# Kernel optimization log

Measured on AMD Instinct MI355X. Metric: run time of the kernel, lower is better.

The kernel has to match this reference:

```python
import jax, jax.numpy as jnp
import numpy as np


def setup_inputs() -> dict:
    key = jax.random.key(0)
    kq, kk, kv = jax.random.split(key, 3)
    B, H, N, D = 2, 16, 2048, 64
    q = jax.random.normal(kq, (B, H, N, D), dtype=jnp.float32)
    k = jax.random.normal(kk, (B, H, N, D), dtype=jnp.float32)
    v = jax.random.normal(kv, (B, H, N, D), dtype=jnp.float32)
    return {"q": q, "k": k, "v": v}


def reference(q, k, v):
    # RBF-kernel causal attention: logits = -relu(||q-k||^2) / sqrt(D)
    B, H, N, D = q.shape
    sm_scale = 1.0 / jnp.sqrt(jnp.asarray(D, dtype=q.dtype))
    q_sq = jnp.sum(q * q, axis=-1)              # [B,H,N]
    k_sq = jnp.sum(k * k, axis=-1)              # [B,H,N]
    qk = jnp.einsum("bhmd,bhnd->bhmn", q, k)    # [B,H,N,N]
    dist_sq = q_sq[..., :, None] + k_sq[..., None, :] - 2.0 * qk
    dist_sq = jnp.maximum(dist_sq, 0.0)         # relu on squared distance
    logits = -dist_sq * sm_scale
    # causal mask: query m attends to keys n <= m
    causal = jnp.tril(jnp.ones((N, N), dtype=bool))
    logits = jnp.where(causal, logits, -jnp.inf)
    p = jax.nn.softmax(logits, axis=-1)
    out = jnp.einsum("bhmn,bhnd->bhmd", p, v)
    return out
```

## Files before the change

kernel.cpp:

```cpp
#include <hip/hip_runtime.h>

#define NN 2048
#define DD 64
#define C1 0.36067376f
#define C1H 0.18033688f

typedef _Float16 h8 __attribute__((ext_vector_type(8)));
typedef _Float16 h4 __attribute__((ext_vector_type(4)));
typedef float f32x16 __attribute__((ext_vector_type(16)));

union H8U4 { h8 v; unsigned u[4]; };

__global__ __launch_bounds__(256) void prep(const float* __restrict__ k,
                                            const float* __restrict__ v,
                                            _Float16* __restrict__ Ks,
                                            _Float16* __restrict__ Vs,
                                            float* __restrict__ hk) {
    __shared__ _Float16 T[128][72];
    const int tb = blockIdx.x, bh = blockIdx.y, tid = threadIdx.x;
    const size_t ibase = (size_t)bh * NN * DD + (size_t)tb * 128 * DD;
    const int lane = tid & 63, ln = lane & 31, lh = lane >> 5;

#pragma unroll
    for (int it = 0; it < 8; ++it) {
        int f = tid + 256 * it;
        int row = f >> 4, c4 = (f & 15) * 4;
        float4 a = *(const float4*)&k[ibase + (size_t)row * DD + c4];
        h4 hv = {(_Float16)a.x, (_Float16)a.y, (_Float16)a.z, (_Float16)a.w};
        *(h4*)&T[row][c4] = hv;
        float s = a.x * a.x + a.y * a.y + a.z * a.z + a.w * a.w;
        s += __shfl_xor(s, 1, 16);
        s += __shfl_xor(s, 2, 16);
        s += __shfl_xor(s, 4, 16);
        s += __shfl_xor(s, 8, 16);
        if ((tid & 15) == 0) hk[bh * NN + tb * 128 + row] = s * C1H;
    }
    __syncthreads();
#pragma unroll
    for (int it = 0; it < 4; ++it) {
        int f2 = tid + 256 * it;
        int combo = f2 >> 6;
        int jl = combo >> 2, c = combo & 3;
        h8 r = *(const h8*)&T[32 * jl + ln][16 * c + 8 * lh];
        *(h8*)&Ks[(size_t)bh * 131072 + (size_t)(4 * tb + jl) * 2048
                  + (size_t)(c * 64 + lane) * 8] = r;
    }
    __syncthreads();

#pragma unroll
    for (int it = 0; it < 8; ++it) {
        int f = tid + 256 * it;
        int row = f >> 4, c4 = (f & 15) * 4;
        float4 a = *(const float4*)&v[ibase + (size_t)row * DD + c4];
        h4 hv = {(_Float16)a.x, (_Float16)a.y, (_Float16)a.z, (_Float16)a.w};
        *(h4*)&T[row][c4] = hv;
    }
    __syncthreads();
#pragma unroll
    for (int it = 0; it < 4; ++it) {
        int f2 = tid + 256 * it;
        int combo = f2 >> 6;
        int jl = combo >> 2, o = (combo >> 1) & 1, c = combo & 1;
        h8 r;
#pragma unroll
        for (int jx = 0; jx < 8; ++jx)
            r[jx] = T[32 * jl + 16 * c + 8 * lh + jx][32 * o + ln];
        *(h8*)&Vs[(size_t)bh * 131072 + (size_t)(4 * tb + jl) * 2048
                  + (size_t)(o * 128 + c * 64 + lane) * 8] = r;
    }
}

__global__ __launch_bounds__(128, 2) void rbf_attn(
    const float* __restrict__ q, const _Float16* __restrict__ Ks,
    const _Float16* __restrict__ Vs, const float* __restrict__ hk,
    float* __restrict__ out)
{
    const int tid = threadIdx.x;
    const int bh = blockIdx.x;
    const int qb = 31 - blockIdx.y;
    const int wv = tid >> 6, lane = tid & 63;
    const int ln = lane & 31, lh = lane >> 5;
    const int jmax = 2 * qb + wv;
    const int qrow = qb * 64 + wv * 32 + ln;
    const size_t fbase = (size_t)bh * NN * DD;

    h8 qf[4];
    {
        const float* qr = q + fbase + (size_t)qrow * DD;
#pragma unroll
        for (int c = 0; c < 4; ++c) {
            float4 a = *(const float4*)&qr[16 * c + 8 * lh];
            float4 b = *(const float4*)&qr[16 * c + 8 * lh + 4];
            qf[c] = h8{(_Float16)a.x, (_Float16)a.y, (_Float16)a.z, (_Float16)a.w,
                       (_Float16)b.x, (_Float16)b.y, (_Float16)b.z, (_Float16)b.w};
        }
    }

    const _Float16* Ksb = Ks + (size_t)bh * 131072;
    const _Float16* Vsb = Vs + (size_t)bh * 131072;
    const float4* hk4 = (const float4*)(hk + bh * NN);
    const int klq = (lh * 32 + ln) * 8;

    f32x16 O0, O1;
#pragma unroll
    for (int r = 0; r < 16; ++r) { O0[r] = 0.f; O1[r] = 0.f; }
    float lsum = 0.f, mrun = -INFINITY;

    auto loadT = [&](int jj, h8 (&kf)[4], h8 (&vf)[4], float4 (&hr)[4]) {
        const _Float16* kp = Ksb + (size_t)jj * 2048 + klq;
        const _Float16* vp = Vsb + (size_t)jj * 2048 + klq;
#pragma unroll
        for (int c = 0; c < 4; ++c) kf[c] = *(const h8*)(kp + c * 512);
#pragma unroll
        for (int oc = 0; oc < 4; ++oc)
            vf[oc] = *(const h8*)(vp + (oc >> 1) * 1024 + (oc & 1) * 512);
#pragma unroll
        for (int g = 0; g < 4; ++g) hr[g] = hk4[jj * 8 + g * 2 + lh];
    };

    auto comp = [&](int jj, h8 (&kf)[4], h8 (&vf)[4], float4 (&hr)[4]) {
        f32x16 S;
#pragma unroll
        for (int r = 0; r < 16; ++r) S[r] = 0.f;
#pragma unroll
        for (int c = 0; c < 4; ++c)
            S = __builtin_amdgcn_mfma_f32_32x32x16_f16(kf[c], qf[c], S, 0, 0, 0);

        const bool diag = (jj == jmax);
        float x[16];
#pragma unroll
        for (int r = 0; r < 16; ++r) {
            const float* hf = (const float*)&hr[r >> 2];
            float xv = fmaf(S[r], C1, -hf[r & 3]);
            if (diag) {
                int keyloc = (r & 3) + 8 * (r >> 2) + 4 * lh;
                if (keyloc > ln) xv = -INFINITY;
            }
            x[r] = xv;
        }
        float mt = x[0];
#pragma unroll
        for (int r = 1; r < 16; ++r) mt = fmaxf(mt, x[r]);
        mt = fmaxf(mt, __shfl_xor(mt, 32));
        if (__ballot(mt > mrun) != 0ull) {
            float mnew = fmaxf(mrun, mt);
            float alpha = __builtin_amdgcn_exp2f(mrun - mnew);
            mrun = mnew;
            lsum *= alpha;
#pragma unroll
            for (int r = 0; r < 16; ++r) { O0[r] *= alpha; O1[r] *= alpha; }
        }
        float p[16], ps = 0.f;
#pragma unroll
        for (int r = 0; r < 16; ++r) {
            p[r] = __builtin_amdgcn_exp2f(x[r] - mrun);
            ps += p[r];
        }
        lsum += ps;

        unsigned pk[8];
#pragma unroll
        for (int hh = 0; hh < 8; ++hh) {
            auto pr = __builtin_amdgcn_cvt_pkrtz(p[2 * hh], p[2 * hh + 1]);
            unsigned pu; __builtin_memcpy(&pu, &pr, 4);
            pk[hh] = pu;
        }
#pragma unroll
        for (int s = 0; s < 2; ++s) {
            unsigned send0 = lh ? pk[4 * s + 0] : pk[4 * s + 2];
            unsigned send1 = lh ? pk[4 * s + 1] : pk[4 * s + 3];
            unsigned r0 = (unsigned)__shfl_xor((int)send0, 32);
            unsigned r1 = (unsigned)__shfl_xor((int)send1, 32);
            H8U4 pb;
            pb.u[0] = lh ? r0 : pk[4 * s + 0];
            pb.u[1] = lh ? r1 : pk[4 * s + 1];
            pb.u[2] = lh ? pk[4 * s + 2] : r0;
            pb.u[3] = lh ? pk[4 * s + 3] : r1;
            O0 = __builtin_amdgcn_mfma_f32_32x32x16_f16(vf[s], pb.v, O0, 0, 0, 0);
            O1 = __builtin_amdgcn_mfma_f32_32x32x16_f16(vf[2 + s], pb.v, O1, 0, 0, 0);
        }
    };

    h8 kfA[4], vfA[4]; float4 hrA[4];
    h8 kfB[4], vfB[4]; float4 hrB[4];
    loadT(0, kfA, vfA, hrA);
    __builtin_amdgcn_sched_barrier(0);
    int jj = 0;
    while (true) {
        if (jj < jmax) loadT(jj + 1, kfB, vfB, hrB);
        __builtin_amdgcn_sched_barrier(0);
        comp(jj, kfA, vfA, hrA);
        __builtin_amdgcn_sched_barrier(0);
        if (++jj > jmax) break;
        if (jj < jmax) loadT(jj + 1, kfA, vfA, hrA);
        __builtin_amdgcn_sched_barrier(0);
        comp(jj, kfB, vfB, hrB);
        __builtin_amdgcn_sched_barrier(0);
        if (++jj > jmax) break;
    }

    float lt = lsum + __shfl_xor(lsum, 32);
    float inv = 1.f / lt;
    size_t ro = fbase + (size_t)qrow * DD;
#pragma unroll
    for (int g = 0; g < 4; ++g) {
        float4 o0 = make_float4(O0[4 * g + 0] * inv, O0[4 * g + 1] * inv,
                                O0[4 * g + 2] * inv, O0[4 * g + 3] * inv);
        *(float4*)&out[ro + 8 * g + 4 * lh] = o0;
        float4 o1 = make_float4(O1[4 * g + 0] * inv, O1[4 * g + 1] * inv,
                                O1[4 * g + 2] * inv, O1[4 * g + 3] * inv);
        *(float4*)&out[ro + 32 + 8 * g + 4 * lh] = o1;
    }
}

extern "C" void kernel_launch(void* const* d_in, const int* in_sizes, int n_in,
                              void* d_out, int out_size, void* d_ws, size_t ws_size,
                              hipStream_t stream) {
    (void)in_sizes; (void)n_in; (void)out_size; (void)ws_size;
    const float* q = (const float*)d_in[0];
    const float* k = (const float*)d_in[1];
    const float* v = (const float*)d_in[2];
    float* out = (float*)d_out;

    float* hk = (float*)d_ws;
    _Float16* Ks = (_Float16*)((char*)d_ws + 262144);
    _Float16* Vs = (_Float16*)((char*)d_ws + 262144 + 8388608);

    prep<<<dim3(16, 32), 256, 0, stream>>>(k, v, Ks, Vs, hk);
    rbf_attn<<<dim3(32, 32), 128, 0, stream>>>(q, Ks, Vs, hk, out);
}
```

Before: 138.4 us.

## Fuse prep and attention into cooperative kernel with grid sync and asm loads

Merges the K/V fp16 conversion prep kernel and the attention kernel into one cooperative launch. Each block prepares a 64-row slice, then all blocks meet at a grid-wide sync before attention, which removes one kernel launch and the gap between launches. Tile loads now go through inline-asm global_load_dwordx4 with explicit vmcnt waits in place of compiler-scheduled loads and sched barriers. The risks are the cost of the grid barrier, the need for all 1024 blocks to be co-resident, and a fallback to two launches if the cooperative launch fails.

```diff
diff --git a/kernel.cpp b/kernel.cpp
--- a/kernel.cpp
+++ b/kernel.cpp
@@ -1,4 +1,7 @@
 #include <hip/hip_runtime.h>
+#include <hip/hip_cooperative_groups.h>
+
+namespace cg = cooperative_groups;
 
 #define NN 2048
 #define DD 64
@@ -7,49 +10,54 @@
 
 typedef _Float16 h8 __attribute__((ext_vector_type(8)));
 typedef _Float16 h4 __attribute__((ext_vector_type(4)));
+typedef float fx4 __attribute__((ext_vector_type(4)));
 typedef float f32x16 __attribute__((ext_vector_type(16)));
 
-union H8U4 { h8 v; unsigned u[4]; };
-
-__global__ __launch_bounds__(256) void prep(const float* __restrict__ k,
-                                            const float* __restrict__ v,
-                                            _Float16* __restrict__ Ks,
-                                            _Float16* __restrict__ Vs,
-                                            float* __restrict__ hk) {
-    __shared__ _Float16 T[128][72];
-    const int tb = blockIdx.x, bh = blockIdx.y, tid = threadIdx.x;
-    const size_t ibase = (size_t)bh * NN * DD + (size_t)tb * 128 * DD;
-    const int lane = tid & 63, ln = lane & 31, lh = lane >> 5;
-
+#define GL4(dst, ap, off) \
+    asm volatile("global_load_dwordx4 %0, %1, off offset:" off \
+                 : "=v"(dst) : "v"(ap))
+
+#define WAITS(cnt, K, V, H) \
+    asm volatile("s_waitcnt vmcnt(" cnt ")" \
+        : "+v"(K[0]), "+v"(K[1]), "+v"(K[2]), "+v"(K[3]), \
+          "+v"(V[0]), "+v"(V[1]), "+v"(V[2]), "+v"(V[3]), \
+          "+v"(H[0]), "+v"(H[1]), "+v"(H[2]), "+v"(H[3]))
+
+__device__ __forceinline__ void prep_phase(
+    int bh, int s, int tid,
+    const float* __restrict__ k, const float* __restrict__ v,
+    _Float16* __restrict__ Ks, _Float16* __restrict__ Vs,
+    float* __restrict__ hkw, _Float16 (*T)[72])
+{
+    const size_t ibase = (size_t)bh * NN * DD + (size_t)s * 64 * DD;
 #pragma unroll
     for (int it = 0; it < 8; ++it) {
-        int f = tid + 256 * it;
+        int f = tid + 128 * it;
         int row = f >> 4, c4 = (f & 15) * 4;
         float4 a = *(const float4*)&k[ibase + (size_t)row * DD + c4];
         h4 hv = {(_Float16)a.x, (_Float16)a.y, (_Float16)a.z, (_Float16)a.w};
         *(h4*)&T[row][c4] = hv;
-        float s = a.x * a.x + a.y * a.y + a.z * a.z + a.w * a.w;
-        s += __shfl_xor(s, 1, 16);
-        s += __shfl_xor(s, 2, 16);
-        s += __shfl_xor(s, 4, 16);
-        s += __shfl_xor(s, 8, 16);
-        if ((tid & 15) == 0) hk[bh * NN + tb * 128 + row] = s * C1H;
+        float sq = a.x * a.x + a.y * a.y + a.z * a.z + a.w * a.w;
+        sq += __shfl_xor(sq, 1, 16);
+        sq += __shfl_xor(sq, 2, 16);
+        sq += __shfl_xor(sq, 4, 16);
+        sq += __shfl_xor(sq, 8, 16);
+        if ((tid & 15) == 0) hkw[bh * NN + s * 64 + row] = sq * C1H;
     }
     __syncthreads();
 #pragma unroll
     for (int it = 0; it < 4; ++it) {
-        int f2 = tid + 256 * it;
-        int combo = f2 >> 6;
-        int jl = combo >> 2, c = combo & 3;
-        h8 r = *(const h8*)&T[32 * jl + ln][16 * c + 8 * lh];
-        *(h8*)&Ks[(size_t)bh * 131072 + (size_t)(4 * tb + jl) * 2048
-                  + (size_t)(c * 64 + lane) * 8] = r;
+        int rec = tid + 128 * it;
+        int tl = rec >> 8, c = (rec >> 6) & 3, lr = rec & 63;
+        int lnr = lr & 31, lhr = lr >> 5;
+        h8 r = *(const h8*)&T[32 * tl + lnr][16 * c + 8 * lhr];
+        *(h8*)&Ks[(size_t)bh * 131072 + (size_t)(s * 2 + tl) * 2048
+                  + (size_t)(c * 64 + lr) * 8] = r;
     }
     __syncthreads();
-
 #pragma unroll
     for (int it = 0; it < 8; ++it) {
-        int f = tid + 256 * it;
+        int f = tid + 128 * it;
         int row = f >> 4, c4 = (f & 15) * 4;
         float4 a = *(const float4*)&v[ibase + (size_t)row * DD + c4];
         h4 hv = {(_Float16)a.x, (_Float16)a.y, (_Float16)a.z, (_Float16)a.w};
@@ -58,26 +66,24 @@
     __syncthreads();
 #pragma unroll
     for (int it = 0; it < 4; ++it) {
-        int f2 = tid + 256 * it;
-        int combo = f2 >> 6;
-        int jl = combo >> 2, o = (combo >> 1) & 1, c = combo & 1;
+        int rec = tid + 128 * it;
+        int tl = rec >> 8, o = (rec >> 7) & 1, c = (rec >> 6) & 1, lr = rec & 63;
+        int lnr = lr & 31, lhr = lr >> 5;
         h8 r;
 #pragma unroll
         for (int jx = 0; jx < 8; ++jx)
-            r[jx] = T[32 * jl + 16 * c + 8 * lh + jx][32 * o + ln];
-        *(h8*)&Vs[(size_t)bh * 131072 + (size_t)(4 * tb + jl) * 2048
-                  + (size_t)(o * 128 + c * 64 + lane) * 8] = r;
-    }
-}
-
-__global__ __launch_bounds__(128, 2) void rbf_attn(
+            r[jx] = T[32 * tl + 16 * c + 8 * lhr + jx][32 * o + lnr];
+        *(h8*)&Vs[(size_t)bh * 131072 + (size_t)(s * 2 + tl) * 2048
+                  + (size_t)(o * 128 + c * 64 + lr) * 8] = r;
+    }
+}
+
+__device__ __forceinline__ void attn_phase(
+    int bh, int qb, int tid,
     const float* __restrict__ q, const _Float16* __restrict__ Ks,
-    const _Float16* __restrict__ Vs, const float* __restrict__ hk,
+    const _Float16* __restrict__ Vs, const float* __restrict__ hkw,
     float* __restrict__ out)
 {
-    const int tid = threadIdx.x;
-    const int bh = blockIdx.x;
-    const int qb = 31 - blockIdx.y;
     const int wv = tid >> 6, lane = tid & 63;
     const int ln = lane & 31, lh = lane >> 5;
     const int jmax = 2 * qb + wv;
@@ -96,51 +102,50 @@
         }
     }
 
-    const _Float16* Ksb = Ks + (size_t)bh * 131072;
-    const _Float16* Vsb = Vs + (size_t)bh * 131072;
-    const float4* hk4 = (const float4*)(hk + bh * NN);
-    const int klq = (lh * 32 + ln) * 8;
+    const unsigned long long kb0 =
+        (unsigned long long)Ks + (size_t)bh * 262144 + (size_t)lane * 16;
+    const unsigned long long vb0 =
+        (unsigned long long)Vs + (size_t)bh * 262144 + (size_t)lane * 16;
+    const unsigned long long hb0 =
+        (unsigned long long)(hkw + bh * NN) + (size_t)lh * 16;
 
     f32x16 O0, O1;
 #pragma unroll
     for (int r = 0; r < 16; ++r) { O0[r] = 0.f; O1[r] = 0.f; }
     float lsum = 0.f, mrun = -INFINITY;
 
-    auto loadT = [&](int jj, h8 (&kf)[4], h8 (&vf)[4], float4 (&hr)[4]) {
-        const _Float16* kp = Ksb + (size_t)jj * 2048 + klq;
-        const _Float16* vp = Vsb + (size_t)jj * 2048 + klq;
-#pragma unroll
-        for (int c = 0; c < 4; ++c) kf[c] = *(const h8*)(kp + c * 512);
-#pragma unroll
-        for (int oc = 0; oc < 4; ++oc)
-            vf[oc] = *(const h8*)(vp + (oc >> 1) * 1024 + (oc & 1) * 512);
-#pragma unroll
-        for (int g = 0; g < 4; ++g) hr[g] = hk4[jj * 8 + g * 2 + lh];
-    };
-
-    auto comp = [&](int jj, h8 (&kf)[4], h8 (&vf)[4], float4 (&hr)[4]) {
+#define ISSUE(jjv, K, V, H) do { \
+        unsigned long long kp = kb0 + (unsigned long long)(jjv) * 4096; \
+        unsigned long long vp = vb0 + (unsigned long long)(jjv) * 4096; \
+        unsigned long long hp = hb0 + (unsigned long long)(jjv) * 128;  \
+        GL4(K[0], kp, "0"); GL4(K[1], kp, "1024"); \
+        GL4(K[2], kp, "2048"); GL4(K[3], kp, "3072"); \
+        GL4(V[0], vp, "0"); GL4(V[1], vp, "1024"); \
+        GL4(V[2], vp, "2048"); GL4(V[3], vp, "3072"); \
+        GL4(H[0], hp, "0"); GL4(H[1], hp, "32"); \
+        GL4(H[2], hp, "64"); GL4(H[3], hp, "96"); \
+    } while (0)
+
+    auto comp = [&](int jj, fx4 (&K)[4], fx4 (&V)[4], fx4 (&H)[4]) {
         f32x16 S;
 #pragma unroll
         for (int r = 0; r < 16; ++r) S[r] = 0.f;
 #pragma unroll
-        for (int c = 0; c < 4; ++c)
-            S = __builtin_amdgcn_mfma_f32_32x32x16_f16(kf[c], qf[c], S, 0, 0, 0);
-
+        for (int c = 0; c < 4; ++c) {
+            h8 kf; __builtin_memcpy(&kf, &K[c], 16);
+            S = __builtin_amdgcn_mfma_f32_32x32x16_f16(kf, qf[c], S, 0, 0, 0);
+        }
         const bool diag = (jj == jmax);
-        float x[16];
 #pragma unroll
         for (int r = 0; r < 16; ++r) {
-            const float* hf = (const float*)&hr[r >> 2];
-            float xv = fmaf(S[r], C1, -hf[r & 3]);
-            if (diag) {
-                int keyloc = (r & 3) + 8 * (r >> 2) + 4 * lh;
-                if (keyloc > ln) xv = -INFINITY;
-            }
-            x[r] = xv;
-        }
-        float mt = x[0];
-#pragma unroll
-        for (int r = 1; r < 16; ++r) mt = fmaxf(mt, x[r]);
+            float hv = ((const float*)&H[r >> 2])[r & 3];
+            float xv = fmaf(S[r], C1, -hv);
+            if (diag && ((r & 3) + 8 * (r >> 2) + 4 * lh > ln)) xv = -INFINITY;
+            S[r] = xv;
+        }
+        float mt = S[0];
+#pragma unroll
+        for (int r = 1; r < 16; ++r) mt = fmaxf(mt, S[r]);
         mt = fmaxf(mt, __shfl_xor(mt, 32));
         if (__ballot(mt > mrun) != 0ull) {
             float mnew = fmaxf(mrun, mt);
@@ -150,54 +155,51 @@
 #pragma unroll
             for (int r = 0; r < 16; ++r) { O0[r] *= alpha; O1[r] *= alpha; }
         }
-        float p[16], ps = 0.f;
-#pragma unroll
-        for (int r = 0; r < 16; ++r) {
-            p[r] = __builtin_amdgcn_exp2f(x[r] - mrun);
-            ps += p[r];
-        }
-        lsum += ps;
-
         unsigned pk[8];
+        float ps = 0.f;
 #pragma unroll
         for (int hh = 0; hh < 8; ++hh) {
-            auto pr = __builtin_amdgcn_cvt_pkrtz(p[2 * hh], p[2 * hh + 1]);
+            float p0 = __builtin_amdgcn_exp2f(S[2 * hh] - mrun);
+            float p1 = __builtin_amdgcn_exp2f(S[2 * hh + 1] - mrun);
+            ps += p0 + p1;
+            auto pr = __builtin_amdgcn_cvt_pkrtz(p0, p1);
             unsigned pu; __builtin_memcpy(&pu, &pr, 4);
             pk[hh] = pu;
         }
+        lsum += ps;
 #pragma unroll
         for (int s = 0; s < 2; ++s) {
             unsigned send0 = lh ? pk[4 * s + 0] : pk[4 * s + 2];
             unsigned send1 = lh ? pk[4 * s + 1] : pk[4 * s + 3];
             unsigned r0 = (unsigned)__shfl_xor((int)send0, 32);
             unsigned r1 = (unsigned)__shfl_xor((int)send1, 32);
-            H8U4 pb;
-            pb.u[0] = lh ? r0 : pk[4 * s + 0];
-            pb.u[1] = lh ? r1 : pk[4 * s + 1];
-            pb.u[2] = lh ? pk[4 * s + 2] : r0;
-            pb.u[3] = lh ? pk[4 * s + 3] : r1;
-            O0 = __builtin_amdgcn_mfma_f32_32x32x16_f16(vf[s], pb.v, O0, 0, 0, 0);
-            O1 = __builtin_amdgcn_mfma_f32_32x32x16_f16(vf[2 + s], pb.v, O1, 0, 0, 0);
+            unsigned pb[4];
+            pb[0] = lh ? r0 : pk[4 * s + 0];
+            pb[1] = lh ? r1 : pk[4 * s + 1];
+            pb[2] = lh ? pk[4 * s + 2] : r0;
+            pb[3] = lh ? pk[4 * s + 3] : r1;
+            h8 pbv; __builtin_memcpy(&pbv, pb, 16);
+            h8 v0; __builtin_memcpy(&v0, &V[s], 16);
+            h8 v1; __builtin_memcpy(&v1, &V[2 + s], 16);
+            O0 = __builtin_amdgcn_mfma_f32_32x32x16_f16(v0, pbv, O0, 0, 0, 0);
+            O1 = __builtin_amdgcn_mfma_f32_32x32x16_f16(v1, pbv, O1, 0, 0, 0);
         }
     };
 
-    h8 kfA[4], vfA[4]; float4 hrA[4];
-    h8 kfB[4], vfB[4]; float4 hrB[4];
-    loadT(0, kfA, vfA, hrA);
-    __builtin_amdgcn_sched_barrier(0);
+    fx4 KA[4], VA[4], HA[4], KB[4], VB[4], HB[4];
+    ISSUE(0, KA, VA, HA);
     int jj = 0;
     while (true) {
-        if (jj < jmax) loadT(jj + 1, kfB, vfB, hrB);
-        __builtin_amdgcn_sched_barrier(0);
-        comp(jj, kfA, vfA, hrA);
-        __builtin_amdgcn_sched_barrier(0);
+        if (jj < jmax) { ISSUE(jj + 1, KB, VB, HB); WAITS("12", KA, VA, HA); }
+        else           { WAITS("0", KA, VA, HA); }
+        comp(jj, KA, VA, HA);
         if (++jj > jmax) break;
-        if (jj < jmax) loadT(jj + 1, kfA, vfA, hrA);
-        __builtin_amdgcn_sched_barrier(0);
-        comp(jj, kfB, vfB, hrB);
-        __builtin_amdgcn_sched_barrier(0);
+        if (jj < jmax) { ISSUE(jj + 1, KA, VA, HA); WAITS("12", KB, VB, HB); }
+        else           { WAITS("0", KB, VB, HB); }
+        comp(jj, KB, VB, HB);
         if (++jj > jmax) break;
     }
+#undef ISSUE
 
     float lt = lsum + __shfl_xor(lsum, 32);
     float inv = 1.f / lt;
@@ -211,6 +213,35 @@
                                 O1[4 * g + 2] * inv, O1[4 * g + 3] * inv);
         *(float4*)&out[ro + 32 + 8 * g + 4 * lh] = o1;
     }
+}
+
+__global__ __launch_bounds__(128, 2) void fused(
+    const float* __restrict__ q, const float* __restrict__ k,
+    const float* __restrict__ v, float* __restrict__ hkw,
+    _Float16* __restrict__ Ks, _Float16* __restrict__ Vs,
+    float* __restrict__ out)
+{
+    __shared__ _Float16 T[64][72];
+    prep_phase(blockIdx.x, blockIdx.y, threadIdx.x, k, v, Ks, Vs, hkw, T);
+    cg::this_grid().sync();
+    attn_phase(blockIdx.x, 31 - blockIdx.y, threadIdx.x, q, Ks, Vs, hkw, out);
+}
+
+__global__ __launch_bounds__(128) void prep_k(
+    const float* __restrict__ k, const float* __restrict__ v,
+    float* __restrict__ hkw, _Float16* __restrict__ Ks,
+    _Float16* __restrict__ Vs)
+{
+    __shared__ _Float16 T[64][72];
+    prep_phase(blockIdx.x, blockIdx.y, threadIdx.x, k, v, Ks, Vs, hkw, T);
+}
+
+__global__ __launch_bounds__(128, 2) void attn_k(
+    const float* __restrict__ q, const _Float16* __restrict__ Ks,
+    const _Float16* __restrict__ Vs, const float* __restrict__ hkw,
+    float* __restrict__ out)
+{
+    attn_phase(blockIdx.x, 31 - blockIdx.y, threadIdx.x, q, Ks, Vs, hkw, out);
 }
 
 extern "C" void kernel_launch(void* const* d_in, const int* in_sizes, int n_in,
@@ -222,10 +253,16 @@
     const float* v = (const float*)d_in[2];
     float* out = (float*)d_out;
 
-    float* hk = (float*)d_ws;
+    float* hkw = (float*)d_ws;
     _Float16* Ks = (_Float16*)((char*)d_ws + 262144);
     _Float16* Vs = (_Float16*)((char*)d_ws + 262144 + 8388608);
 
-    prep<<<dim3(16, 32), 256, 0, stream>>>(k, v, Ks, Vs, hk);
-    rbf_attn<<<dim3(32, 32), 128, 0, stream>>>(q, Ks, Vs, hk, out);
-}
+    void* args[7] = {(void*)&q, (void*)&k, (void*)&v, (void*)&hkw,
+                     (void*)&Ks, (void*)&Vs, (void*)&out};
+    hipError_t e = hipLaunchCooperativeKernel((const void*)fused, dim3(32, 32),
+                                              dim3(128, 1, 1), args, 0, stream);
+    if (e != hipSuccess) {
+        prep_k<<<dim3(32, 32), 128, 0, stream>>>(k, v, hkw, Ks, Vs);
+        attn_k<<<dim3(32, 32), 128, 0, stream>>>(q, Ks, Vs, hkw, out);
+    }
+}
```

After: 276.6 us. +99.9%, slower.
